# Kernel tuning notes

Measured on AMD Instinct MI355X. Metric: run time of the kernel, lower is better.

Reference implementation:

```python
import jax, jax.numpy as jnp
import numpy as np

B, S, D, H = 4, 2048, 1024, 16
DH = D // H  # 64, head_embed_dim


def setup_inputs() -> dict:
    key = jax.random.key(0)
    ks = jax.random.split(key, 12)
    scale = 1.0 / np.sqrt(D)
    inp = {
        "query": jax.random.normal(ks[0], (B, S, D), jnp.float32),
        "key": jax.random.normal(ks[1], (B, S, D), jnp.float32),
        "value": jax.random.normal(ks[2], (B, S, D), jnp.float32),
        "key_padding_mask": jax.random.randint(ks[3], (B, S), 0, 2).astype(bool),
        # Linear params stored as [in, out] (math-equivalent to torch's [out,in].T)
        "Wq": jax.random.normal(ks[4], (D, H * DH), jnp.float32) * scale,
        "bq": jnp.zeros((H * DH,), jnp.float32),
        "Wk": jax.random.normal(ks[5], (D, H * DH), jnp.float32) * scale,
        "bk": jnp.zeros((H * DH,), jnp.float32),
        "Wv": jax.random.normal(ks[6], (D, H * DH), jnp.float32) * scale,
        "bv": jnp.zeros((H * DH,), jnp.float32),
        "Wo": jax.random.normal(ks[7], (H * DH, D), jnp.float32) * scale,
        "bo": jnp.zeros((D,), jnp.float32),
    }
    return inp


def reference(query, key, value, key_padding_mask, Wq, bq, Wk, bk, Wv, bv, Wo, bo):
    b, nq, _ = query.shape
    nk = key.shape[-2]
    # QKV projections -> [B, H, S, DH]
    q = (query @ Wq + bq).reshape(b, nq, H, DH).transpose(0, 2, 1, 3)
    k = (key @ Wk + bk).reshape(b, nk, H, DH).transpose(0, 2, 1, 3)
    v = (value @ Wv + bv).reshape(b, nk, H, DH).transpose(0, 2, 1, 3)
    # scaled dot-product scores [B, H, Sq, Sk]
    scores = jnp.einsum("bhqd,bhkd->bhqk", q, k) / np.sqrt(DH)
    # key_padding_mask broadcast over heads and query positions; True = masked
    mask = key_padding_mask[:, None, None, :]
    scores = jnp.where(mask, -jnp.inf, scores)
    w = jax.nn.softmax(scores, axis=-1)
    attn = jnp.einsum("bhqk,bhkd->bhqd", w, v)
    attn = attn.transpose(0, 2, 1, 3).reshape(b, nq, H * DH)
    return attn @ Wo + bo
```

## Files before the change

### kernel.cpp

```cpp
#include <hip/hip_runtime.h>
#include <hip/hip_bf16.h>

#define Bc 4
#define Sc 2048
#define Dc 1024
#define Hc 16
#define DHc 64

typedef unsigned short u16;
typedef unsigned int u32;
typedef __attribute__((ext_vector_type(8))) short bfrag;
typedef __attribute__((ext_vector_type(4))) float f32x4;

#define SCALE_Q 0.18033688011112042f

#if __has_builtin(__builtin_amdgcn_exp2f)
#define EXP2(x) __builtin_amdgcn_exp2f(x)
#else
#define EXP2(x) exp2f(x)
#endif

__device__ __forceinline__ u16 f2bf(float f) {
  u32 u = __float_as_uint(f);
  return (u16)((u + 0x7fffu + ((u >> 16) & 1u)) >> 16);
}
__device__ __forceinline__ float bf2f(u16 h) { return __uint_as_float(((u32)h) << 16); }

__device__ __forceinline__ u32 pkbf(float a, float b) {
  union { __hip_bfloat162 h; u32 u; } c;
  c.h = __float22bfloat162_rn(make_float2(a, b));
  return c.u;
}

union FB { bfrag f; u32 w[4]; };

#if __has_builtin(__builtin_amdgcn_permlane32_swap) && __has_builtin(__builtin_amdgcn_permlane16_swap)
typedef __attribute__((ext_vector_type(2))) unsigned int u32x2;
__device__ __forceinline__ void pl32swap(u32& x, u32& y) {
  u32x2 r = __builtin_amdgcn_permlane32_swap(x, y, false, false);
  x = r.x; y = r.y;
}
__device__ __forceinline__ void pl16swap(u32& x, u32& y) {
  u32x2 r = __builtin_amdgcn_permlane16_swap(x, y, false, false);
  x = r.x; y = r.y;
}
#else
__device__ __forceinline__ void pl32swap(u32& x, u32& y) {
  asm volatile("v_permlane32_swap_b32 %0, %1" : "+v"(x), "+v"(y));
}
__device__ __forceinline__ void pl16swap(u32& x, u32& y) {
  asm volatile("v_permlane16_swap_b32 %0, %1" : "+v"(x), "+v"(y));
}
#endif

__device__ __forceinline__ void gl_lds16(const u16* g, u16* l) {
  __builtin_amdgcn_global_load_lds(
      (const __attribute__((address_space(1))) unsigned int*)g,
      (__attribute__((address_space(3))) unsigned int*)l, 16, 0, 0);
}

__global__ __launch_bounds__(256) void prep_kernel(
    const void* __restrict__ qsrc, const void* __restrict__ mask,
    const void* __restrict__ bq, const void* __restrict__ bk,
    const void* __restrict__ bv, const void* __restrict__ bo,
    int* __restrict__ flags, float* __restrict__ maskf, float* __restrict__ biasf) {
  __shared__ int c_bf, c_ni, c_nf;
  const int tid = threadIdx.x;
  if (tid == 0) { c_bf = 0; c_ni = 0; c_nf = 0; }
  __syncthreads();
  u32 w = ((const u32*)qsrc)[tid];
  int e = (int)((w >> 7) & 0xffu);
  if (e >= 118 && e <= 130) atomicAdd(&c_bf, 1);
  int ni = 0, nf = 0;
  for (int i = tid; i < 2048; i += 256) {
    u32 v = ((const u32*)mask)[i];
    if (v > 1u) ni = 1;
    if (v != 0u && v != 0x3f800000u) nf = 1;
  }
  if (ni) atomicAdd(&c_ni, 1);
  if (nf) atomicAdd(&c_nf, 1);
  __syncthreads();
  const int isbf = (c_bf > 128) ? 1 : 0;
  const int layout = (c_ni == 0) ? 0 : ((c_nf == 0) ? 2 : 1);
  if (tid == 0) { flags[0] = isbf; flags[1] = layout; }
  for (int i = tid; i < Bc * Sc; i += 256) {
    int mv;
    if (layout == 0) mv = ((const int*)mask)[i];
    else if (layout == 1) mv = (int)((const unsigned char*)mask)[i];
    else mv = (((const u32*)mask)[i] != 0u) ? 1 : 0;
    maskf[i] = mv ? -1e30f : 0.0f;
  }
  const void* bs[4] = {bq, bk, bv, bo};
  for (int j = 0; j < 4; ++j) {
    const void* bp = bs[j];
    float sc = (j == 0) ? SCALE_Q : 1.0f;
    for (int i = tid; i < Dc; i += 256)
      biasf[j * Dc + i] = (isbf ? bf2f(((const u16*)bp)[i]) : ((const float*)bp)[i]) * sc;
  }
}

__global__ __launch_bounds__(256) void cvt3(
    const void* __restrict__ s0, const void* __restrict__ s1, const void* __restrict__ s2,
    u16* __restrict__ d0, u16* __restrict__ d1, u16* __restrict__ d2,
    const int* __restrict__ flags) {
  const void* s = blockIdx.y == 0 ? s0 : (blockIdx.y == 1 ? s1 : s2);
  u16* d = blockIdx.y == 0 ? d0 : (blockIdx.y == 1 ? d1 : d2);
  size_t e = ((size_t)blockIdx.x * 256 + threadIdx.x) * 8;
  if (flags[0]) {
    *(uint4*)(d + e) = *(const uint4*)((const u16*)s + e);
  } else {
    const float* p = (const float*)s + e;
    float4 f0 = *(const float4*)p, f1 = *(const float4*)(p + 4);
    uint4 st;
    st.x = pkbf(f0.x, f0.y); st.y = pkbf(f0.z, f0.w);
    st.z = pkbf(f1.x, f1.y); st.w = pkbf(f1.z, f1.w);
    *(uint4*)(d + e) = st;
  }
}

__global__ __launch_bounds__(256) void transpose_all(
    const void* __restrict__ W0, const void* __restrict__ W1,
    const void* __restrict__ W2, const void* __restrict__ W3,
    u16* __restrict__ D0, u16* __restrict__ D1, u16* __restrict__ D2,
    u16* __restrict__ D3, const int* __restrict__ flags) {
  __shared__ short ts[64][72];
  const int z = blockIdx.z;
  const void* W = z == 0 ? W0 : (z == 1 ? W1 : (z == 2 ? W2 : W3));
  u16* Wt = z == 0 ? D0 : (z == 1 ? D1 : (z == 2 ? D2 : D3));
  const float scale = (z == 0) ? SCALE_Q : 1.0f;
  const int r0 = blockIdx.y * 64, c0 = blockIdx.x * 64;
  const int isbf = flags[0];
  for (int i = 0; i < 2; ++i) {
    int ch = threadIdx.x + i * 256;
    int r = ch >> 3, c = (ch & 7) * 8;
    bfrag pk;
    if (isbf) {
      uint4 v = *(const uint4*)((const u16*)W + (size_t)(r0 + r) * Dc + c0 + c);
      const u16* pv = (const u16*)&v;
      for (int j = 0; j < 8; ++j) pk[j] = (short)f2bf(bf2f(pv[j]) * scale);
    } else {
      const float* p = (const float*)W + (size_t)(r0 + r) * Dc + c0 + c;
      float4 f0 = *(const float4*)p, f1 = *(const float4*)(p + 4);
      pk[0] = (short)f2bf(f0.x * scale); pk[1] = (short)f2bf(f0.y * scale);
      pk[2] = (short)f2bf(f0.z * scale); pk[3] = (short)f2bf(f0.w * scale);
      pk[4] = (short)f2bf(f1.x * scale); pk[5] = (short)f2bf(f1.y * scale);
      pk[6] = (short)f2bf(f1.z * scale); pk[7] = (short)f2bf(f1.w * scale);
    }
    *(bfrag*)(&ts[r][c]) = pk;
  }
  __syncthreads();
  for (int i = 0; i < 2; ++i) {
    int ch = threadIdx.x + i * 256;
    int n = ch >> 3, k = (ch & 7) * 8;
    u16 tmp[8] __attribute__((aligned(16)));
    for (int j = 0; j < 8; ++j) tmp[j] = (u16)ts[k + j][n];
    *(uint4*)(Wt + (size_t)(c0 + n) * Dc + r0 + k) = *(const uint4*)tmp;
  }
}

#define BM 128
#define BN 128
#define BK 32

#define GEMM_STAGE(bufI)                                                          \
  {                                                                               \
    gl_lds16(bgp0, &Bs[bufI][wave * 16][0]);                                      \
    gl_lds16(bgp1, &Bs[bufI][wave * 16 + 64][0]);                                 \
    bgp0 += BK; bgp1 += BK;                                                       \
    if (a_bf) {                                                                   \
      gl_lds16(agp0, &As[bufI][wave * 16][0]);                                    \
      gl_lds16(agp1, &As[bufI][wave * 16 + 64][0]);                               \
      agp0 += BK; agp1 += BK;                                                     \
    } else {                                                                      \
      for (int i_ = 0; i_ < 2; ++i_) {                                            \
        int ch_ = tid + i_ * 256;                                                 \
        int r_ = ch_ >> 2, kc_ = (ch_ & 3) * 8;                                   \
        const float* p_ = (const float*)Araw + (size_t)(bm0 + r_) * K + ksf + kc_;\
        float4 f0_ = *(const float4*)p_, f1_ = *(const float4*)(p_ + 4);          \
        uint4 st_;                                                                \
        st_.x = pkbf(f0_.x, f0_.y); st_.y = pkbf(f0_.z, f0_.w);                   \
        st_.z = pkbf(f1_.x, f1_.y); st_.w = pkbf(f1_.z, f1_.w);                   \
        *(uint4*)(&As[bufI][r_][kc_]) = st_;                                      \
      }                                                                           \
    }                                                                             \
    ksf += BK;                                                                    \
  }

__global__ __launch_bounds__(256) void gemm_bt(
    const void* __restrict__ Araw, const u16* __restrict__ Bt,
    const float* __restrict__ bias, void* __restrict__ Cout, u16* __restrict__ VtOut,
    const int* __restrict__ flags, int M, int N, int K,
    int a_mode , int c_mode ,
    int qkv ) {
  __shared__ __align__(16) u16 As[2][BM][BK];
  __shared__ __align__(16) u16 Bs[2][BN][BK];
  if (qkv) {
    const int z = blockIdx.z;
    Araw = (const void*)((const u16*)Araw + (size_t)z * Bc * Sc * Dc);
    Bt += (size_t)z * Dc * Dc;
    bias += z * Dc;
    if (z == 2) { c_mode = 2; Cout = (void*)VtOut; }
    else Cout = (void*)((u16*)Cout + (size_t)z * Bc * Sc * Dc);
  }
  const int tid = threadIdx.x;
  const int lane = tid & 63, wave = tid >> 6;
  const int lr = lane & 15, lq = lane >> 4;
  const int ntiles = N >> 7;
  const int band = (M >> 7) >> 3;
  const int L = blockIdx.x;
  const int mt = (L & 7) * band + ((L >> 3) / ntiles);
  const int nt = (L >> 3) % ntiles;
  const int bm0 = mt * BM, bn0 = nt * BN;
  const int wm = (wave >> 1) * 64, wn = (wave & 1) * 64;
  const int a_bf = a_mode ? 1 : flags[0];
  const int srow = lane >> 2;
  const int schunk = lane & 3;
  const u16* bgp0 = Bt + (size_t)(bn0 + wave * 16 + srow) * K + schunk * 8;
  const u16* bgp1 = bgp0 + (size_t)64 * K;
  const u16* agp0 = (const u16*)Araw + (size_t)(bm0 + wave * 16 + srow) * K + schunk * 8;
  const u16* agp1 = agp0 + (size_t)64 * K;
  int ksf = 0;
  f32x4 acc[4][4] = {};
  GEMM_STAGE(0);
  __syncthreads();
  const int NIT = K / BK;
#pragma unroll 2
  for (int it = 0; it < NIT; ++it) {
    const int p = it & 1;
    if (it + 1 < NIT) { GEMM_STAGE(p ^ 1); }
    bfrag af[4], bf[4];
    for (int mi = 0; mi < 4; ++mi) af[mi] = *(const bfrag*)(&As[p][wm + mi * 16 + lr][lq * 8]);
    for (int nj = 0; nj < 4; ++nj) bf[nj] = *(const bfrag*)(&Bs[p][wn + nj * 16 + lr][lq * 8]);
    for (int mi = 0; mi < 4; ++mi)
      for (int nj = 0; nj < 4; ++nj)
        acc[mi][nj] = __builtin_amdgcn_mfma_f32_16x16x32_bf16(af[mi], bf[nj], acc[mi][nj], 0, 0, 0);
    __syncthreads();
  }
  float bcol[4];
  for (int nj = 0; nj < 4; ++nj) bcol[nj] = bias[bn0 + wn + nj * 16 + lr];
  if (c_mode == 2) {
    u16* VT = (u16*)Cout;
    for (int mi = 0; mi < 4; ++mi)
      for (int nj = 0; nj < 4; ++nj) {
        int row = bm0 + wm + mi * 16 + lq * 4;
        int col = bn0 + wn + nj * 16 + lr;
        float v0 = acc[mi][nj][0] + bcol[nj], v1 = acc[mi][nj][1] + bcol[nj];
        float v2 = acc[mi][nj][2] + bcol[nj], v3 = acc[mi][nj][3] + bcol[nj];
        uint2 st;
        st.x = (u32)f2bf(v0) | ((u32)f2bf(v1) << 16);
        st.y = (u32)f2bf(v2) | ((u32)f2bf(v3) << 16);
        size_t drow = (size_t)((row >> 11) * Hc + (col >> 6)) * DHc + (col & 63);
        *(uint2*)(VT + drow * Sc + (row & (Sc - 1))) = st;
      }
  } else {
    const int outbf = (c_mode == 0) ? 1 : flags[0];
    for (int mi = 0; mi < 4; ++mi)
      for (int r = 0; r < 4; ++r) {
        int row = bm0 + wm + mi * 16 + lq * 4 + r;
        for (int nj = 0; nj < 4; ++nj) {
          int col = bn0 + wn + nj * 16 + lr;
          float v = acc[mi][nj][r] + bcol[nj];
          if (outbf) ((u16*)Cout)[(size_t)row * N + col] = f2bf(v);
          else ((float*)Cout)[(size_t)row * N + col] = v;
        }
      }
  }
}

__global__ __launch_bounds__(256) void attn_kernel(
    const u16* __restrict__ Q, const u16* __restrict__ K,
    const u16* __restrict__ Vt, const float* __restrict__ maskf,
    u16* __restrict__ Aout) {
  __shared__ __align__(16) u16 Ks[2][64][64];
  __shared__ __align__(16) u16 Vts[2][64][64];
  __shared__ float maskL[Sc];
  const int tid = threadIdx.x;
  const int lane = tid & 63, wave = tid >> 6;
  const int lr = lane & 15, lq = lane >> 4;
  const int bh = blockIdx.x;
  const int b = bh >> 4, h = bh & 15;
  const int q0 = blockIdx.y * 128;
  const int wq = wave * 32;
  const int rr0 = wave * 16 + (lane >> 3);
  const int rr1 = rr0 + 8;
  const int cc = lane & 7;
  const u16* kg0 = K + (size_t)(b * Sc + rr0) * Dc + h * DHc + ((cc ^ (rr0 & 7)) * 8);
  const u16* kg1 = K + (size_t)(b * Sc + rr1) * Dc + h * DHc + ((cc ^ (rr1 & 7)) * 8);
  const u16* vg0 = Vt + (size_t)((b * Hc + h) * DHc + rr0) * Sc + ((cc ^ (rr0 & 7)) * 8);
  const u16* vg1 = Vt + (size_t)((b * Hc + h) * DHc + rr1) * Sc + ((cc ^ (rr1 & 7)) * 8);
#define ATTN_STAGE(bufI)                                      \
  {                                                           \
    gl_lds16(kg0, &Ks[bufI][wave * 16][0]);                   \
    gl_lds16(kg1, &Ks[bufI][wave * 16 + 8][0]);               \
    gl_lds16(vg0, &Vts[bufI][wave * 16][0]);                  \
    gl_lds16(vg1, &Vts[bufI][wave * 16 + 8][0]);              \
    kg0 += (size_t)64 * Dc; kg1 += (size_t)64 * Dc;           \
    vg0 += 64; vg1 += 64;                                     \
  }
  bfrag qf[2][2];
  for (int mi = 0; mi < 2; ++mi)
    for (int ks = 0; ks < 2; ++ks)
      qf[mi][ks] = *(const bfrag*)(Q + (size_t)(b * Sc + q0 + wq + mi * 16 + lr) * Dc +
                                   h * DHc + ks * 32 + lq * 8);
  f32x4 oacc[2][4] = {};
  f32x4 oext[2] = {};
  FB ones;
  ones.w[0] = 0x3F803F80u; ones.w[1] = 0x3F803F80u; ones.w[2] = 0x3F803F80u; ones.w[3] = 0x3F803F80u;
  ATTN_STAGE(0);
  {
    const float4* ms = (const float4*)(maskf + b * Sc);
    for (int i = tid; i < Sc / 4; i += 256) ((float4*)maskL)[i] = ms[i];
  }
  __syncthreads();
  const int lrx = lr & 7;
#pragma unroll 2
  for (int kt = 0; kt < Sc / 64; ++kt) {
    const int p = kt & 1;
    if (kt + 1 < Sc / 64) { ATTN_STAGE(p ^ 1); }
    f32x4 sacc[2][4];
    for (int nk = 0; nk < 4; ++nk) {
      f32x4 mk = *(const f32x4*)(&maskL[kt * 64 + nk * 16 + lq * 4]);
      sacc[0][nk] = mk;
      sacc[1][nk] = mk;
    }
    for (int nk = 0; nk < 4; ++nk) {
      const int kr = nk * 16 + lr;
      bfrag kf0 = *(const bfrag*)(&Ks[p][kr][(lq ^ lrx) * 8]);
      bfrag kf1 = *(const bfrag*)(&Ks[p][kr][((4 + lq) ^ lrx) * 8]);
      for (int mi = 0; mi < 2; ++mi) {
        sacc[mi][nk] = __builtin_amdgcn_mfma_f32_16x16x32_bf16(kf0, qf[mi][0], sacc[mi][nk], 0, 0, 0);
        sacc[mi][nk] = __builtin_amdgcn_mfma_f32_16x16x32_bf16(kf1, qf[mi][1], sacc[mi][nk], 0, 0, 0);
      }
    }
    for (int c = 0; c < 2; ++c) {
      FB pb[2];
      for (int mi = 0; mi < 2; ++mi) {
        const f32x4 s0 = sacc[mi][2 * c];
        const f32x4 s1 = sacc[mi][2 * c + 1];
        u32 w0 = pkbf(EXP2(s0[0]), EXP2(s0[1]));
        u32 w1 = pkbf(EXP2(s0[2]), EXP2(s0[3]));
        u32 w2 = pkbf(EXP2(s1[0]), EXP2(s1[1]));
        u32 w3 = pkbf(EXP2(s1[2]), EXP2(s1[3]));
        pl32swap(w0, w2); pl16swap(w0, w2);
        pl32swap(w1, w3); pl16swap(w1, w3);
        pb[mi].w[0] = w0; pb[mi].w[1] = w1; pb[mi].w[2] = w2; pb[mi].w[3] = w3;
        oext[mi] = __builtin_amdgcn_mfma_f32_16x16x32_bf16(ones.f, pb[mi].f, oext[mi], 0, 0, 0);
      }
      for (int nd = 0; nd < 4; ++nd) {
        const int dr = nd * 16 + lr;
        const bfrag vb = *(const bfrag*)(&Vts[p][dr][((4 * c + lq) ^ lrx) * 8]);
        oacc[0][nd] = __builtin_amdgcn_mfma_f32_16x16x32_bf16(vb, pb[0].f, oacc[0][nd], 0, 0, 0);
        oacc[1][nd] = __builtin_amdgcn_mfma_f32_16x16x32_bf16(vb, pb[1].f, oacc[1][nd], 0, 0, 0);
      }
    }
    __syncthreads();
  }
  for (int mi = 0; mi < 2; ++mi) {
    float inv = 1.0f / oext[mi][0];
    u16* rowp = Aout + (size_t)(b * Sc + q0 + wq + mi * 16 + lr) * Dc + h * DHc;
    for (int nd = 0; nd < 4; ++nd) {
      float o0 = oacc[mi][nd][0] * inv, o1 = oacc[mi][nd][1] * inv;
      float o2 = oacc[mi][nd][2] * inv, o3 = oacc[mi][nd][3] * inv;
      uint2 st;
      st.x = pkbf(o0, o1);
      st.y = pkbf(o2, o3);
      *(uint2*)(rowp + nd * 16 + lq * 4) = st;
    }
  }
}

extern "C" void kernel_launch(void* const* d_in, const int* in_sizes, int n_in,
                              void* d_out, int out_size, void* d_ws, size_t ws_size,
                              hipStream_t stream) {
  (void)in_sizes; (void)n_in; (void)out_size;
  char* ws = (char*)d_ws;
  int* flags = (int*)ws;
  float* maskf = (float*)(ws + 256);
  float* biasf = (float*)(ws + 256 + Bc * Sc * 4);
  u16* WqT = (u16*)(ws + 65536);
  u16* WkT = WqT + (size_t)Dc * Dc;
  u16* WvT = WkT + (size_t)Dc * Dc;
  u16* WoT = WvT + (size_t)Dc * Dc;
  u16* Qb  = WoT + (size_t)Dc * Dc;
  u16* Kb  = Qb + (size_t)Bc * Sc * Dc;
  u16* Vb  = Kb + (size_t)Bc * Sc * Dc;
  u16* Vtb = Vb + (size_t)Bc * Sc * Dc;
  u16* Ab  = Vtb + (size_t)Bc * Sc * Dc;
  u16* qbf = Ab + (size_t)Bc * Sc * Dc;
  u16* kbf = qbf + (size_t)Bc * Sc * Dc;
  u16* vbf = kbf + (size_t)Bc * Sc * Dc;
  const size_t need = (size_t)((char*)(vbf + (size_t)Bc * Sc * Dc) - ws);
  const bool have_cvt = ws_size >= need;

  prep_kernel<<<1, 256, 0, stream>>>(d_in[0], d_in[3], d_in[5], d_in[7], d_in[9], d_in[11],
                                     flags, maskf, biasf);
  transpose_all<<<dim3(16, 16, 4), 256, 0, stream>>>(d_in[4], d_in[6], d_in[8], d_in[10],
                                                     WqT, WkT, WvT, WoT, flags);
  const int nblk = (Bc * Sc / BM) * (Dc / BN);
  if (have_cvt) {
    cvt3<<<dim3(4096, 3), 256, 0, stream>>>(d_in[0], d_in[1], d_in[2], qbf, kbf, vbf, flags);
    gemm_bt<<<dim3(nblk, 1, 3), 256, 0, stream>>>(qbf, WqT, biasf, Qb, Vtb, flags,
                                                  Bc * Sc, Dc, Dc, 1, 0, 1);
  } else {
    gemm_bt<<<nblk, 256, 0, stream>>>(d_in[0], WqT, biasf, Qb, nullptr, flags,
                                      Bc * Sc, Dc, Dc, 0, 0, 0);
    gemm_bt<<<nblk, 256, 0, stream>>>(d_in[1], WkT, biasf + Dc, Kb, nullptr, flags,
                                      Bc * Sc, Dc, Dc, 0, 0, 0);
    gemm_bt<<<nblk, 256, 0, stream>>>(d_in[2], WvT, biasf + 2 * Dc, Vtb, nullptr, flags,
                                      Bc * Sc, Dc, Dc, 0, 2, 0);
  }
  attn_kernel<<<dim3(64, 16), 256, 0, stream>>>(Qb, Kb, Vtb, maskf, Ab);
  gemm_bt<<<nblk, 256, 0, stream>>>(Ab, WoT, biasf + 3 * Dc, d_out, nullptr, flags,
                                    Bc * Sc, Dc, Dc, 1, 1, 0);
}
```

Baseline: 384.0 us.

## Software-pipeline attention loop: overlap next tile's QK^T with current PV

Restructures the attention key loop into a two-stage software pipeline. The S = QK^T MFMAs for tile kt+1 are issued alongside the exp/PV work for tile kt, and K and V loads into LDS are staged separately so K arrives one tile ahead. The goal is to hide MFMA and exp latency and LDS load waits by interleaving independent work. In exchange it keeps two score accumulator sets live, which raises register pressure, and it adds more barriers per iteration.

```diff
diff --git a/kernel.cpp b/kernel.cpp
--- a/kernel.cpp
+++ b/kernel.cpp
@@ -288,13 +288,16 @@
   const u16* kg1 = K + (size_t)(b * Sc + rr1) * Dc + h * DHc + ((cc ^ (rr1 & 7)) * 8);
   const u16* vg0 = Vt + (size_t)((b * Hc + h) * DHc + rr0) * Sc + ((cc ^ (rr0 & 7)) * 8);
   const u16* vg1 = Vt + (size_t)((b * Hc + h) * DHc + rr1) * Sc + ((cc ^ (rr1 & 7)) * 8);
-#define ATTN_STAGE(bufI)                                      \
+#define STAGE_K(bufI)                                         \
   {                                                           \
     gl_lds16(kg0, &Ks[bufI][wave * 16][0]);                   \
     gl_lds16(kg1, &Ks[bufI][wave * 16 + 8][0]);               \
+    kg0 += (size_t)64 * Dc; kg1 += (size_t)64 * Dc;           \
+  }
+#define STAGE_V(bufI)                                         \
+  {                                                           \
     gl_lds16(vg0, &Vts[bufI][wave * 16][0]);                  \
     gl_lds16(vg1, &Vts[bufI][wave * 16 + 8][0]);              \
-    kg0 += (size_t)64 * Dc; kg1 += (size_t)64 * Dc;           \
     vg0 += 64; vg1 += 64;                                     \
   }
   bfrag qf[2][2];
@@ -306,55 +309,75 @@
   f32x4 oext[2] = {};
   FB ones;
   ones.w[0] = 0x3F803F80u; ones.w[1] = 0x3F803F80u; ones.w[2] = 0x3F803F80u; ones.w[3] = 0x3F803F80u;
-  ATTN_STAGE(0);
+  const int lrx = lr & 7;
+  const int NT = Sc / 64;
+  f32x4 saccA[2][4], saccB[2][4];
+
+#define SBLOCK(KB, ktt, DST)                                                                  \
+  {                                                                                           \
+    for (int nk = 0; nk < 4; ++nk) {                                                          \
+      const int kr = nk * 16 + lr;                                                            \
+      bfrag kf0 = *(const bfrag*)(&Ks[KB][kr][(lq ^ lrx) * 8]);                               \
+      bfrag kf1 = *(const bfrag*)(&Ks[KB][kr][((4 + lq) ^ lrx) * 8]);                         \
+      f32x4 mk = *(const f32x4*)(&maskL[(ktt) * 64 + nk * 16 + lq * 4]);                      \
+      for (int mi = 0; mi < 2; ++mi) {                                                        \
+        f32x4 t = __builtin_amdgcn_mfma_f32_16x16x32_bf16(kf0, qf[mi][0], mk, 0, 0, 0);       \
+        DST[mi][nk] = __builtin_amdgcn_mfma_f32_16x16x32_bf16(kf1, qf[mi][1], t, 0, 0, 0);    \
+      }                                                                                       \
+    }                                                                                         \
+  }
+
+#define PVBLOCK(VB, SRC)                                                                      \
+  {                                                                                           \
+    for (int c = 0; c < 2; ++c) {                                                             \
+      FB pb[2];                                                                               \
+      for (int mi = 0; mi < 2; ++mi) {                                                        \
+        const f32x4 s0 = SRC[mi][2 * c];                                                      \
+        const f32x4 s1 = SRC[mi][2 * c + 1];                                                  \
+        u32 w0 = pkbf(EXP2(s0[0]), EXP2(s0[1]));                                              \
+        u32 w1 = pkbf(EXP2(s0[2]), EXP2(s0[3]));                                              \
+        u32 w2 = pkbf(EXP2(s1[0]), EXP2(s1[1]));                                              \
+        u32 w3 = pkbf(EXP2(s1[2]), EXP2(s1[3]));                                              \
+        pl32swap(w0, w2); pl16swap(w0, w2);                                                   \
+        pl32swap(w1, w3); pl16swap(w1, w3);                                                   \
+        pb[mi].w[0] = w0; pb[mi].w[1] = w1; pb[mi].w[2] = w2; pb[mi].w[3] = w3;               \
+      }                                                                                       \
+      for (int nd = 0; nd < 4; ++nd) {                                                        \
+        const int dr = nd * 16 + lr;                                                          \
+        const bfrag vb = *(const bfrag*)(&Vts[VB][dr][((4 * c + lq) ^ lrx) * 8]);             \
+        oacc[0][nd] = __builtin_amdgcn_mfma_f32_16x16x32_bf16(vb, pb[0].f, oacc[0][nd], 0, 0, 0); \
+        oacc[1][nd] = __builtin_amdgcn_mfma_f32_16x16x32_bf16(vb, pb[1].f, oacc[1][nd], 0, 0, 0); \
+      }                                                                                       \
+      oext[0] = __builtin_amdgcn_mfma_f32_16x16x32_bf16(ones.f, pb[0].f, oext[0], 0, 0, 0);   \
+      oext[1] = __builtin_amdgcn_mfma_f32_16x16x32_bf16(ones.f, pb[1].f, oext[1], 0, 0, 0);   \
+    }                                                                                         \
+  }
+
+  STAGE_K(0);
+  STAGE_V(0);
   {
     const float4* ms = (const float4*)(maskf + b * Sc);
     for (int i = tid; i < Sc / 4; i += 256) ((float4*)maskL)[i] = ms[i];
   }
   __syncthreads();
-  const int lrx = lr & 7;
-#pragma unroll 2
-  for (int kt = 0; kt < Sc / 64; ++kt) {
-    const int p = kt & 1;
-    if (kt + 1 < Sc / 64) { ATTN_STAGE(p ^ 1); }
-    f32x4 sacc[2][4];
-    for (int nk = 0; nk < 4; ++nk) {
-      f32x4 mk = *(const f32x4*)(&maskL[kt * 64 + nk * 16 + lq * 4]);
-      sacc[0][nk] = mk;
-      sacc[1][nk] = mk;
+  STAGE_K(1);
+  SBLOCK(0, 0, saccA);
+
+  for (int kt = 0; kt < NT; kt += 2) {
+    __syncthreads();
+    if (kt + 2 < NT) STAGE_K(0);
+    STAGE_V(1);
+    SBLOCK(1, kt + 1, saccB);
+    PVBLOCK(0, saccA);
+    __syncthreads();
+    if (kt + 3 < NT) STAGE_K(1);
+    if (kt + 2 < NT) {
+      STAGE_V(0);
+      SBLOCK(0, kt + 2, saccA);
     }
-    for (int nk = 0; nk < 4; ++nk) {
-      const int kr = nk * 16 + lr;
-      bfrag kf0 = *(const bfrag*)(&Ks[p][kr][(lq ^ lrx) * 8]);
-      bfrag kf1 = *(const bfrag*)(&Ks[p][kr][((4 + lq) ^ lrx) * 8]);
-      for (int mi = 0; mi < 2; ++mi) {
-        sacc[mi][nk] = __builtin_amdgcn_mfma_f32_16x16x32_bf16(kf0, qf[mi][0], sacc[mi][nk], 0, 0, 0);
-        sacc[mi][nk] = __builtin_amdgcn_mfma_f32_16x16x32_bf16(kf1, qf[mi][1], sacc[mi][nk], 0, 0, 0);
-      }
-    }
-    for (int c = 0; c < 2; ++c) {
-      FB pb[2];
-      for (int mi = 0; mi < 2; ++mi) {
-        const f32x4 s0 = sacc[mi][2 * c];
-        const f32x4 s1 = sacc[mi][2 * c + 1];
-        u32 w0 = pkbf(EXP2(s0[0]), EXP2(s0[1]));
-        u32 w1 = pkbf(EXP2(s0[2]), EXP2(s0[3]));
-        u32 w2 = pkbf(EXP2(s1[0]), EXP2(s1[1]));
-        u32 w3 = pkbf(EXP2(s1[2]), EXP2(s1[3]));
-        pl32swap(w0, w2); pl16swap(w0, w2);
-        pl32swap(w1, w3); pl16swap(w1, w3);
-        pb[mi].w[0] = w0; pb[mi].w[1] = w1; pb[mi].w[2] = w2; pb[mi].w[3] = w3;
-        oext[mi] = __builtin_amdgcn_mfma_f32_16x16x32_bf16(ones.f, pb[mi].f, oext[mi], 0, 0, 0);
-      }
-      for (int nd = 0; nd < 4; ++nd) {
-        const int dr = nd * 16 + lr;
-        const bfrag vb = *(const bfrag*)(&Vts[p][dr][((4 * c + lq) ^ lrx) * 8]);
-        oacc[0][nd] = __builtin_amdgcn_mfma_f32_16x16x32_bf16(vb, pb[0].f, oacc[0][nd], 0, 0, 0);
-        oacc[1][nd] = __builtin_amdgcn_mfma_f32_16x16x32_bf16(vb, pb[1].f, oacc[1][nd], 0, 0, 0);
-      }
-    }
-    __syncthreads();
-  }
+    PVBLOCK(1, saccB);
+  }
+
   for (int mi = 0; mi < 2; ++mi) {
     float inv = 1.0f / oext[mi][0];
     u16* rowp = Aout + (size_t)(b * Sc + q0 + wq + mi * 16 + lr) * Dc + h * DHc;
@@ -367,6 +390,10 @@
       *(uint2*)(rowp + nd * 16 + lq * 4) = st;
     }
   }
+#undef STAGE_K
+#undef STAGE_V
+#undef SBLOCK
+#undef PVBLOCK
 }
 
 extern "C" void kernel_launch(void* const* d_in, const int* in_sizes, int n_in,
```

Measured after the change: 382.3 us. About the same (-0.4%).

## Double attention query tile per wave and use hardware exp/bf16-pack instructions

Applied to the files above, without the earlier changes.

Each wave now handles 64 query rows instead of 32, so every K/V tile staged in LDS is reused across twice as many MFMA operations and the grid halves along the query dimension. The mask is fed straight in as the MFMA accumulator seed, and the row-sum MFMAs are moved after the PV MFMAs. Exp2 and bf16 packing are replaced with inline v_exp_f32 and v_cvt_pk_bf16_f32 asm, including in the V-transpose GEMM epilogue. The larger accumulator set raises register pressure, which can lower occupancy, and the halved grid gives 512 blocks for the attention kernel.

```diff
diff --git a/kernel.cpp b/kernel.cpp
--- a/kernel.cpp
+++ b/kernel.cpp
@@ -14,11 +14,12 @@
 
 #define SCALE_Q 0.18033688011112042f
 
-#if __has_builtin(__builtin_amdgcn_exp2f)
-#define EXP2(x) __builtin_amdgcn_exp2f(x)
-#else
-#define EXP2(x) exp2f(x)
-#endif
+__device__ __forceinline__ float exp2_hw(float x) {
+  float r;
+  asm("v_exp_f32 %0, %1" : "=v"(r) : "v"(x));
+  return r;
+}
+#define EXP2(x) exp2_hw(x)
 
 __device__ __forceinline__ u16 f2bf(float f) {
   u32 u = __float_as_uint(f);
@@ -27,9 +28,9 @@
 __device__ __forceinline__ float bf2f(u16 h) { return __uint_as_float(((u32)h) << 16); }
 
 __device__ __forceinline__ u32 pkbf(float a, float b) {
-  union { __hip_bfloat162 h; u32 u; } c;
-  c.h = __float22bfloat162_rn(make_float2(a, b));
-  return c.u;
+  u32 r;
+  asm("v_cvt_pk_bf16_f32 %0, %1, %2" : "=v"(r) : "v"(a), "v"(b));
+  return r;
 }
 
 union FB { bfrag f; u32 w[4]; };
@@ -247,8 +248,8 @@
         float v0 = acc[mi][nj][0] + bcol[nj], v1 = acc[mi][nj][1] + bcol[nj];
         float v2 = acc[mi][nj][2] + bcol[nj], v3 = acc[mi][nj][3] + bcol[nj];
         uint2 st;
-        st.x = (u32)f2bf(v0) | ((u32)f2bf(v1) << 16);
-        st.y = (u32)f2bf(v2) | ((u32)f2bf(v3) << 16);
+        st.x = pkbf(v0, v1);
+        st.y = pkbf(v2, v3);
         size_t drow = (size_t)((row >> 11) * Hc + (col >> 6)) * DHc + (col & 63);
         *(uint2*)(VT + drow * Sc + (row & (Sc - 1))) = st;
       }
@@ -279,8 +280,8 @@
   const int lr = lane & 15, lq = lane >> 4;
   const int bh = blockIdx.x;
   const int b = bh >> 4, h = bh & 15;
-  const int q0 = blockIdx.y * 128;
-  const int wq = wave * 32;
+  const int q0 = blockIdx.y * 256;
+  const int wq = wave * 64;
   const int rr0 = wave * 16 + (lane >> 3);
   const int rr1 = rr0 + 8;
   const int cc = lane & 7;
@@ -288,7 +289,7 @@
   const u16* kg1 = K + (size_t)(b * Sc + rr1) * Dc + h * DHc + ((cc ^ (rr1 & 7)) * 8);
   const u16* vg0 = Vt + (size_t)((b * Hc + h) * DHc + rr0) * Sc + ((cc ^ (rr0 & 7)) * 8);
   const u16* vg1 = Vt + (size_t)((b * Hc + h) * DHc + rr1) * Sc + ((cc ^ (rr1 & 7)) * 8);
-#define ATTN_STAGE(bufI)                                      \
+#define STAGE_KV(bufI)                                        \
   {                                                           \
     gl_lds16(kg0, &Ks[bufI][wave * 16][0]);                   \
     gl_lds16(kg1, &Ks[bufI][wave * 16 + 8][0]);               \
@@ -297,44 +298,48 @@
     kg0 += (size_t)64 * Dc; kg1 += (size_t)64 * Dc;           \
     vg0 += 64; vg1 += 64;                                     \
   }
-  bfrag qf[2][2];
-  for (int mi = 0; mi < 2; ++mi)
+  bfrag qf[4][2];
+#pragma unroll
+  for (int mi = 0; mi < 4; ++mi)
+#pragma unroll
     for (int ks = 0; ks < 2; ++ks)
       qf[mi][ks] = *(const bfrag*)(Q + (size_t)(b * Sc + q0 + wq + mi * 16 + lr) * Dc +
                                    h * DHc + ks * 32 + lq * 8);
-  f32x4 oacc[2][4] = {};
-  f32x4 oext[2] = {};
+  f32x4 oacc[4][4] = {};
+  f32x4 oext[4] = {};
   FB ones;
   ones.w[0] = 0x3F803F80u; ones.w[1] = 0x3F803F80u; ones.w[2] = 0x3F803F80u; ones.w[3] = 0x3F803F80u;
-  ATTN_STAGE(0);
+  const int lrx = lr & 7;
+  const int NT = Sc / 64;
+
+  STAGE_KV(0);
   {
     const float4* ms = (const float4*)(maskf + b * Sc);
     for (int i = tid; i < Sc / 4; i += 256) ((float4*)maskL)[i] = ms[i];
   }
   __syncthreads();
-  const int lrx = lr & 7;
-#pragma unroll 2
-  for (int kt = 0; kt < Sc / 64; ++kt) {
+
+  for (int kt = 0; kt < NT; ++kt) {
     const int p = kt & 1;
-    if (kt + 1 < Sc / 64) { ATTN_STAGE(p ^ 1); }
-    f32x4 sacc[2][4];
-    for (int nk = 0; nk < 4; ++nk) {
-      f32x4 mk = *(const f32x4*)(&maskL[kt * 64 + nk * 16 + lq * 4]);
-      sacc[0][nk] = mk;
-      sacc[1][nk] = mk;
-    }
+    if (kt + 1 < NT) { STAGE_KV(p ^ 1); }
+    f32x4 sacc[4][4];
+#pragma unroll
     for (int nk = 0; nk < 4; ++nk) {
       const int kr = nk * 16 + lr;
-      bfrag kf0 = *(const bfrag*)(&Ks[p][kr][(lq ^ lrx) * 8]);
-      bfrag kf1 = *(const bfrag*)(&Ks[p][kr][((4 + lq) ^ lrx) * 8]);
-      for (int mi = 0; mi < 2; ++mi) {
-        sacc[mi][nk] = __builtin_amdgcn_mfma_f32_16x16x32_bf16(kf0, qf[mi][0], sacc[mi][nk], 0, 0, 0);
-        sacc[mi][nk] = __builtin_amdgcn_mfma_f32_16x16x32_bf16(kf1, qf[mi][1], sacc[mi][nk], 0, 0, 0);
+      const bfrag kf0 = *(const bfrag*)(&Ks[p][kr][(lq ^ lrx) * 8]);
+      const bfrag kf1 = *(const bfrag*)(&Ks[p][kr][((4 + lq) ^ lrx) * 8]);
+      const f32x4 mk = *(const f32x4*)(&maskL[kt * 64 + nk * 16 + lq * 4]);
+#pragma unroll
+      for (int mi = 0; mi < 4; ++mi) {
+        f32x4 t = __builtin_amdgcn_mfma_f32_16x16x32_bf16(kf0, qf[mi][0], mk, 0, 0, 0);
+        sacc[mi][nk] = __builtin_amdgcn_mfma_f32_16x16x32_bf16(kf1, qf[mi][1], t, 0, 0, 0);
       }
     }
+#pragma unroll
     for (int c = 0; c < 2; ++c) {
-      FB pb[2];
-      for (int mi = 0; mi < 2; ++mi) {
+      FB pb[4];
+#pragma unroll
+      for (int mi = 0; mi < 4; ++mi) {
         const f32x4 s0 = sacc[mi][2 * c];
         const f32x4 s1 = sacc[mi][2 * c + 1];
         u32 w0 = pkbf(EXP2(s0[0]), EXP2(s0[1]));
@@ -344,20 +349,27 @@
         pl32swap(w0, w2); pl16swap(w0, w2);
         pl32swap(w1, w3); pl16swap(w1, w3);
         pb[mi].w[0] = w0; pb[mi].w[1] = w1; pb[mi].w[2] = w2; pb[mi].w[3] = w3;
-        oext[mi] = __builtin_amdgcn_mfma_f32_16x16x32_bf16(ones.f, pb[mi].f, oext[mi], 0, 0, 0);
       }
+#pragma unroll
       for (int nd = 0; nd < 4; ++nd) {
         const int dr = nd * 16 + lr;
         const bfrag vb = *(const bfrag*)(&Vts[p][dr][((4 * c + lq) ^ lrx) * 8]);
-        oacc[0][nd] = __builtin_amdgcn_mfma_f32_16x16x32_bf16(vb, pb[0].f, oacc[0][nd], 0, 0, 0);
-        oacc[1][nd] = __builtin_amdgcn_mfma_f32_16x16x32_bf16(vb, pb[1].f, oacc[1][nd], 0, 0, 0);
+#pragma unroll
+        for (int mi = 0; mi < 4; ++mi)
+          oacc[mi][nd] = __builtin_amdgcn_mfma_f32_16x16x32_bf16(vb, pb[mi].f, oacc[mi][nd], 0, 0, 0);
       }
+#pragma unroll
+      for (int mi = 0; mi < 4; ++mi)
+        oext[mi] = __builtin_amdgcn_mfma_f32_16x16x32_bf16(ones.f, pb[mi].f, oext[mi], 0, 0, 0);
     }
     __syncthreads();
   }
-  for (int mi = 0; mi < 2; ++mi) {
+
+#pragma unroll
+  for (int mi = 0; mi < 4; ++mi) {
     float inv = 1.0f / oext[mi][0];
     u16* rowp = Aout + (size_t)(b * Sc + q0 + wq + mi * 16 + lr) * Dc + h * DHc;
+#pragma unroll
     for (int nd = 0; nd < 4; ++nd) {
       float o0 = oacc[mi][nd][0] * inv, o1 = oacc[mi][nd][1] * inv;
       float o2 = oacc[mi][nd][2] * inv, o3 = oacc[mi][nd][3] * inv;
@@ -367,6 +379,7 @@
       *(uint2*)(rowp + nd * 16 + lq * 4) = st;
     }
   }
+#undef STAGE_KV
 }
 
 extern "C" void kernel_launch(void* const* d_in, const int* in_sizes, int n_in,
@@ -409,7 +422,7 @@
     gemm_bt<<<nblk, 256, 0, stream>>>(d_in[2], WvT, biasf + 2 * Dc, Vtb, nullptr, flags,
                                       Bc * Sc, Dc, Dc, 0, 2, 0);
   }
-  attn_kernel<<<dim3(64, 16), 256, 0, stream>>>(Qb, Kb, Vtb, maskf, Ab);
+  attn_kernel<<<dim3(64, 8), 256, 0, stream>>>(Qb, Kb, Vtb, maskf, Ab);
   gemm_bt<<<nblk, 256, 0, stream>>>(Ab, WoT, biasf + 3 * Dc, d_out, nullptr, flags,
                                     Bc * Sc, Dc, Dc, 1, 1, 0);
 }
```

Result: slower. 409.5 us (+6.7%).
